# Performance work log

Hardware: AMD Instinct MI355X
Metric: run time of the kernel (lower is better)

The kernel has to match this reference:

```python
import jax, jax.numpy as jnp
import numpy as np

N_TOKEN = 100000
D = 512
CUTOFFS = [10000, 20000, 50000, N_TOKEN]
CUTOFF_ENDS = [0] + CUTOFFS
N_CLUSTERS = 3
SHORTLIST = 10000
HEAD_SIZE = SHORTLIST + N_CLUSTERS  # 10003
CL_ROOT = [5, 17, 123, 10005, 20007, 50011]
# per-cluster relative root indices (predict_root=False masks roots)
CL_ROOT_REL = []
for i in range(len(CUTOFFS)):
    l, r = CUTOFF_ENDS[i], CUTOFF_ENDS[i + 1]
    CL_ROOT_REL.append([j - l for j in CL_ROOT if l <= j < r])


def _mask_cols(logit, idxs):
    if idxs:
        return logit.at[:, jnp.asarray(idxs)].set(-jnp.inf)
    return logit


def setup_inputs() -> dict:
    key = jax.random.key(0)
    ks = jax.random.split(key, 6)
    return {
        "hidden": jax.random.normal(ks[0], (2048, D), dtype=jnp.float32),
        "weight": jax.random.normal(ks[1], (N_TOKEN, D), dtype=jnp.float32) * 0.02,
        "bias": jax.random.normal(ks[2], (N_TOKEN,), dtype=jnp.float32) * 0.02,
        "cluster_weight": jax.random.normal(ks[3], (N_CLUSTERS, D), dtype=jnp.float32) * 0.02,
        "cluster_bias": jax.random.normal(ks[4], (N_CLUSTERS,), dtype=jnp.float32) * 0.02,
        "target": jax.random.randint(ks[5], (2048,), 0, N_TOKEN, dtype=jnp.int64),
    }


def reference(hidden, weight, bias, cluster_weight, cluster_bias, target):
    # head: shortlist vocab rows + cluster rows
    head_w = jnp.concatenate([weight[:SHORTLIST], cluster_weight], axis=0)  # [HEAD_SIZE, D]
    head_b = jnp.concatenate([bias[:SHORTLIST], cluster_bias], axis=0)
    head_logit = hidden @ head_w.T + head_b                                 # [N, HEAD_SIZE]
    head_logit = _mask_cols(head_logit, CL_ROOT_REL[0])
    head_lp = jax.nn.log_softmax(head_logit, axis=1)

    # cluster 0: direct gather from head log-probs
    mask0 = target < CUTOFFS[0]
    t0 = jnp.clip(target, 0, HEAD_SIZE - 1)
    lp0 = jnp.take_along_axis(head_lp, t0[:, None], axis=1)[:, 0]
    nll = jnp.where(mask0, -lp0, jnp.zeros_like(lp0))

    # tail clusters: dense per-cluster logits for all tokens, select by mask
    for i in range(1, len(CUTOFFS)):
        l, r = CUTOFF_ENDS[i], CUTOFF_ENDS[i + 1]
        tail_logit = hidden @ weight[l:r].T + bias[l:r]                     # [N, r-l]
        tail_logit = _mask_cols(tail_logit, CL_ROOT_REL[i])
        tail_lp = jax.nn.log_softmax(tail_logit, axis=1)
        t_i = jnp.clip(target - l, 0, r - l - 1)
        lp_tail = jnp.take_along_axis(tail_lp, t_i[:, None], axis=1)[:, 0]
        # note: torch indexes head column -i, i.e. HEAD_SIZE - i
        lp_i = head_lp[:, HEAD_SIZE - i] + lp_tail
        mask_i = (target >= l) & (target < r)
        nll = jnp.where(mask_i, -lp_i, nll)
    return nll
```

## Files before the change

### kernel.cpp

```cpp
#include <hip/hip_runtime.h>
#include <math.h>

#define NTOK   2048
#define D      512
#define NV     100000
#define LOG2E  1.44269504f

typedef __attribute__((ext_vector_type(8)))  short bf16x8;
typedef __attribute__((ext_vector_type(16))) float f32x16;


#define WS_FRAGS 0u
#define WS_LISTS 8388608u
#define WS_PART  8421376u
#define WS_CUR   14843904u
#define WS_PAD   14843920u
#define WS_CL    14843936u
#define WS_TGT   14868512u
#define WS_ACC   14876704u

__device__ __forceinline__ int cluster_of(int t){
  return (t < 10000) ? 0 : (t < 20000) ? 1 : (t < 50000) ? 2 : 3;
}
__device__ __forceinline__ bool is_root(int c){
  return c==5 || c==17 || c==123 || c==10005 || c==20007 || c==50011;
}
__device__ __forceinline__ unsigned short f2bf(float f){
  unsigned int u = __float_as_uint(f);
  u += 0x7fffu + ((u >> 16) & 1u);
  return (unsigned short)(u >> 16);
}
__device__ __forceinline__ float bf2f(unsigned short u){
  unsigned int v = ((unsigned int)u) << 16;
  return __uint_as_float(v);
}
__device__ __forceinline__ float fexp2(float x){
#if __has_builtin(__builtin_amdgcn_exp2f)
  return __builtin_amdgcn_exp2f(x);
#else
  return exp2f(x);
#endif
}

__global__ void k_token_logits(const float* __restrict__ hidden,
                               const float* __restrict__ weight,
                               const float* __restrict__ bias,
                               const float* __restrict__ cw,
                               const float* __restrict__ cb,
                               const int*   __restrict__ target,
                               float* __restrict__ cl_out,
                               float* __restrict__ tgt_out,
                               int*   __restrict__ lists,
                               int*   __restrict__ cursors)
{
  int wave = threadIdx.x >> 6;
  int lane = threadIdx.x & 63;
  int n = blockIdx.x * 4 + wave;
  if (n >= NTOK) return;
  const float* h = hidden + (size_t)n * D + lane * 8;
  int t = target[n];
  const float* wt = weight + (size_t)t * D + lane * 8;
  float hv[8];
  #pragma unroll
  for (int i = 0; i < 8; ++i) hv[i] = h[i];
  float acc[4] = {0.f, 0.f, 0.f, 0.f};
  #pragma unroll
  for (int j = 0; j < 3; ++j){
    const float* cwj = cw + j * D + lane * 8;
    float s = 0.f;
    #pragma unroll
    for (int i = 0; i < 8; ++i) s += hv[i] * cwj[i];
    acc[j] = s;
  }
  {
    float s = 0.f;
    #pragma unroll
    for (int i = 0; i < 8; ++i) s += hv[i] * wt[i];
    acc[3] = s;
  }
  #pragma unroll
  for (int m = 1; m < 64; m <<= 1){
    #pragma unroll
    for (int j = 0; j < 4; ++j) acc[j] += __shfl_xor(acc[j], m, 64);
  }
  if (lane == 0){
    cl_out[n*3+0] = acc[0] + cb[0];
    cl_out[n*3+1] = acc[1] + cb[1];
    cl_out[n*3+2] = acc[2] + cb[2];
    float tg = acc[3] + bias[t];
    if (is_root(t)) tg = -INFINITY;
    tgt_out[n] = tg;
    lists[n] = n;
    int c = cluster_of(t);
    if (c > 0){
      int pos = atomicAdd(cursors + c, 1);
      lists[c * 2048 + pos] = n;
    }
  }
}

__global__ void k_pad_lists(int* __restrict__ lists, const int* __restrict__ cursors,
                            int* __restrict__ padded)
{
  if (threadIdx.x == 0) padded[0] = NTOK;
  for (int s = 1; s < 4; ++s){
    int c = cursors[s];
    int p = (c + 255) & ~255;
    if (threadIdx.x == 0) padded[s] = p;
    for (int i = c + threadIdx.x; i < p; i += blockDim.x)
      lists[s * 2048 + i] = NTOK;
  }
}

__global__ void k_build_frags(const float* __restrict__ hidden,
                              const int*   __restrict__ lists,
                              const int*   __restrict__ padded,
                              unsigned short* __restrict__ frags)
{
  int tg   = blockIdx.x * 256 + threadIdx.x;
  int seg  = tg >> 16;
  int s    = tg & 65535;
  int lane = s & 63;
  int ks0  = (s >> 6) & 15;
  int mf   = s >> 10;
  int row  = mf * 32 + (lane & 31);
  if (row >= padded[seg]) return;
  int token = lists[seg * 2048 + row];
  #pragma unroll
  for (int p = 0; p < 2; ++p){
    int ks = ks0 + p * 16;
    unsigned int w[4];
    if (token < NTOK){
      const float* h = hidden + (size_t)token * D + ks * 16 + (lane >> 5) * 8;
      #pragma unroll
      for (int i = 0; i < 4; ++i){
        unsigned short lo = f2bf(h[2*i]   * LOG2E);
        unsigned short hi = f2bf(h[2*i+1] * LOG2E);
        w[i] = (unsigned int)lo | ((unsigned int)hi << 16);
      }
    } else {
      w[0] = w[1] = w[2] = w[3] = 0u;
    }
    size_t off = ((size_t)seg * 2048 * 512) + (((size_t)(mf * 32 + ks)) * 64 + lane) * 8;
    uint4 val; val.x = w[0]; val.y = w[1]; val.z = w[2]; val.w = w[3];
    *(uint4*)(frags + off) = val;
  }
}

__device__ __forceinline__ void epi2(const f32x16& a, const f32x16& b, int r0,
                                     int lane, unsigned short* __restrict__ pp)
{
  float s = 0.f;
  #pragma unroll
  for (int r = 0; r < 16; ++r) s += fexp2(a[r]) + fexp2(b[r]);
  s += __shfl_xor(s, 32, 64);
  if (lane < 32)
    pp[r0 + lane] = f2bf(s);
}

__global__ __launch_bounds__(512, 4)
void k_gemm(const unsigned short* __restrict__ frags,
            const float* __restrict__ weight,
            const float* __restrict__ bias,
            const int*   __restrict__ padded,
            unsigned short* __restrict__ partials)
{
  __shared__ unsigned short Bs[528 * 64];

  int bid = blockIdx.x;
  int seg, strip0, colstart, colend;
  if      (bid < 157) { seg = 0; strip0 = 0;    colstart = 0;     colend = 10000;  }
  else if (bid < 314) { seg = 1; strip0 = 157;  colstart = 10000; colend = 20000;  }
  else if (bid < 783) { seg = 2; strip0 = 314;  colstart = 20000; colend = 50000;  }
  else                { seg = 3; strip0 = 783;  colstart = 50000; colend = 100000; }
  int col_base = colstart + (bid - strip0) * 64;

  int tid   = threadIdx.x;
  int wave  = tid >> 6;
  int lane  = tid & 63;
  int hi    = lane >> 5;
  int M = padded[seg];
  const unsigned short* fseg = frags + (size_t)seg * 2048 * 512;
  unsigned short* pp = partials + (size_t)bid * 2048;

  for (int it = 0; it < 16; ++it){
    int id  = it * 512 + tid;
    int col = id >> 7;
    int k0  = (id & 127) * 4;
    int cg  = col_base + col;
    float4 v = make_float4(0.f, 0.f, 0.f, 0.f);
    if (cg < colend) v = *(const float4*)(weight + (size_t)cg * D + k0);
    unsigned int lo  = (unsigned int)f2bf(v.x) | ((unsigned int)f2bf(v.y) << 16);
    unsigned int hi2 = (unsigned int)f2bf(v.z) | ((unsigned int)f2bf(v.w) << 16);
    int ks = k0 >> 4, bhi = (k0 >> 3) & 1, j0 = k0 & 7;
    int off = ks * 2048 + (col >> 5) * 1024 + bhi * 512 + (col & 31) * 16 + j0 * 2;
    off ^= ((ks & 3) << 5) ^ (bhi << 4);
    uint2 pk; pk.x = lo; pk.y = hi2;
    *(uint2*)((char*)Bs + off) = pk;
  }
  if (tid < 256){
    int col = tid >> 2;
    int q   = tid & 3;
    int bhi = q >> 1;
    int j0  = (q & 1) * 4;
    int cg  = col_base + col;
    unsigned int x = 0u;
    if (bhi == 0 && j0 == 0){
      float bv = (cg < colend && !is_root(cg)) ? bias[cg] * LOG2E : -INFINITY;
      x = (unsigned int)f2bf(bv);
    }
    int off = 32 * 2048 + (col >> 5) * 1024 + bhi * 512 + (col & 31) * 16 + j0 * 2;
    off ^= ((32 & 3) << 5) ^ (bhi << 4);
    uint2 pk; pk.x = x; pk.y = 0u;
    *(uint2*)((char*)Bs + off) = pk;
  }
  __syncthreads();

  const char* bsc = (const char*)Bs;
  int roff = (lane * 16) ^ (hi << 4);

  bf16x8 ones;
  #pragma unroll
  for (int j = 0; j < 8; ++j) ones[j] = (short)0x3F80;

  for (int m0 = 0; m0 < M; m0 += 512){
    int r0 = m0 + wave * 64;
    if (r0 < M){
      f32x16 acc00, acc01, acc10, acc11;
      #pragma unroll
      for (int i = 0; i < 16; ++i){ acc00[i]=0.f; acc01[i]=0.f; acc10[i]=0.f; acc11[i]=0.f; }

      const unsigned short* pa0 = fseg + (size_t)(r0 >> 5) * 16384 + (size_t)lane * 8;
      const unsigned short* pa1 = pa0 + 16384;

      __builtin_amdgcn_s_setprio(1);
      #pragma unroll 4
      for (int ks = 0; ks < 32; ++ks){
        bf16x8 a0 = *(const bf16x8*)(pa0 + ks * 512);
        bf16x8 a1 = *(const bf16x8*)(pa1 + ks * 512);
        int kb = ks * 2048 + (roff ^ ((ks & 3) << 5));
        bf16x8 b0 = *(const bf16x8*)(bsc + kb);
        bf16x8 b1 = *(const bf16x8*)(bsc + kb + 1024);
        acc00 = __builtin_amdgcn_mfma_f32_32x32x16_bf16(b0, a0, acc00, 0, 0, 0);
        acc01 = __builtin_amdgcn_mfma_f32_32x32x16_bf16(b1, a0, acc01, 0, 0, 0);
        acc10 = __builtin_amdgcn_mfma_f32_32x32x16_bf16(b0, a1, acc10, 0, 0, 0);
        acc11 = __builtin_amdgcn_mfma_f32_32x32x16_bf16(b1, a1, acc11, 0, 0, 0);
      }
      {
        int kb32 = 32 * 2048 + roff;
        bf16x8 bb0 = *(const bf16x8*)(bsc + kb32);
        bf16x8 bb1 = *(const bf16x8*)(bsc + kb32 + 1024);
        acc00 = __builtin_amdgcn_mfma_f32_32x32x16_bf16(bb0, ones, acc00, 0, 0, 0);
        acc01 = __builtin_amdgcn_mfma_f32_32x32x16_bf16(bb1, ones, acc01, 0, 0, 0);
        acc10 = __builtin_amdgcn_mfma_f32_32x32x16_bf16(bb0, ones, acc10, 0, 0, 0);
        acc11 = __builtin_amdgcn_mfma_f32_32x32x16_bf16(bb1, ones, acc11, 0, 0, 0);
      }
      __builtin_amdgcn_s_setprio(0);
      epi2(acc00, acc01, r0,      lane, pp);
      epi2(acc10, acc11, r0 + 32, lane, pp);
    }
  }
}

__global__ void k_reduce(const unsigned short* __restrict__ partials,
                         const int*   __restrict__ lists,
                         const int*   __restrict__ padded,
                         float* __restrict__ acc_out)
{
  int b   = blockIdx.x;
  int seg = b >> 3;
  int row = (b & 7) * 256 + threadIdx.x;
  if (row >= padded[seg]) return;
  int base, cnt;
  if      (seg == 0){ base = 0;   cnt = 157; }
  else if (seg == 1){ base = 157; cnt = 157; }
  else if (seg == 2){ base = 314; cnt = 469; }
  else              { base = 783; cnt = 782; }
  float s = 0.f;
  int j = 0;
  for (; j + 4 <= cnt; j += 4){
    s += bf2f(partials[(size_t)(base + j    ) * 2048 + row]);
    s += bf2f(partials[(size_t)(base + j + 1) * 2048 + row]);
    s += bf2f(partials[(size_t)(base + j + 2) * 2048 + row]);
    s += bf2f(partials[(size_t)(base + j + 3) * 2048 + row]);
  }
  for (; j < cnt; ++j) s += bf2f(partials[(size_t)(base + j) * 2048 + row]);
  int token = lists[seg * 2048 + row];
  if (token < NTOK) acc_out[seg * 2049 + token] = s;
}

__global__ void k_finalize(const float* __restrict__ accs,
                           const float* __restrict__ cl,
                           const float* __restrict__ tgt,
                           const int*   __restrict__ target,
                           float* __restrict__ out)
{
  int n = blockIdx.x * blockDim.x + threadIdx.x;
  if (n >= NTOK) return;
  int c = cluster_of(target[n]);
  float e0 = __expf(cl[n*3+0]), e1 = __expf(cl[n*3+1]), e2 = __expf(cl[n*3+2]);
  float head_lse = __logf(accs[n] + e0 + e1 + e2);
  float nll;
  if (c == 0){
    nll = head_lse - tgt[n];
  } else {
    float tail_lse = __logf(accs[c * 2049 + n]);
    nll = head_lse + tail_lse - cl[n*3 + (3 - c)] - tgt[n];
  }
  out[n] = nll;
}

extern "C" void kernel_launch(void* const* d_in, const int* in_sizes, int n_in,
                              void* d_out, int out_size, void* d_ws, size_t ws_size,
                              hipStream_t stream)
{
  (void)in_sizes; (void)n_in; (void)out_size; (void)ws_size;
  const float* hidden = (const float*)d_in[0];
  const float* weight = (const float*)d_in[1];
  const float* bias   = (const float*)d_in[2];
  const float* cw     = (const float*)d_in[3];
  const float* cb     = (const float*)d_in[4];
  const int*   target = (const int*)d_in[5];
  float* out = (float*)d_out;
  char*  ws  = (char*)d_ws;

  unsigned short* frags    = (unsigned short*)(ws + WS_FRAGS);
  int*   lists    = (int*)(ws + WS_LISTS);
  unsigned short* partials = (unsigned short*)(ws + WS_PART);
  int*   cursors  = (int*)(ws + WS_CUR);
  int*   padded   = (int*)(ws + WS_PAD);
  float* cl       = (float*)(ws + WS_CL);
  float* tgt      = (float*)(ws + WS_TGT);
  float* acc      = (float*)(ws + WS_ACC);

  hipMemsetAsync(ws + WS_CUR, 0, 16, stream);

  k_token_logits<<<512, 256, 0, stream>>>(hidden, weight, bias, cw, cb, target,
                                          cl, tgt, lists, cursors);
  k_pad_lists   <<<1,   256, 0, stream>>>(lists, cursors, padded);
  k_build_frags <<<1024,256, 0, stream>>>(hidden, lists, padded, frags);
  k_gemm        <<<1565,512, 0, stream>>>(frags, weight, bias, padded, partials);
  k_reduce      <<<32,  256, 0, stream>>>(partials, lists, padded, acc);
  k_finalize    <<<8,   256, 0, stream>>>(acc, cl, tgt, target, out);
}
```

Measured before the change: 226.8 us.

## Switch GEMM operands from bf16 to fp8 e4m3 MFMA

Converts both the hidden-state fragments and the weight tile in shared memory to software-encoded fp8 (e4m3) and uses the fp8 32x32x16 MFMA instead of bf16. This halves the fragment and LDS footprint and is meant to use the higher fp8 matrix throughput. The fragment and LDS layouts are rebuilt without the XOR swizzle, and the masked bias becomes -448 instead of -inf. The risk is a large accuracy loss in the log-sum-exp from fp8 rounding and the finite mask value.

```diff
diff --git a/kernel.cpp b/kernel.cpp
--- a/kernel.cpp
+++ b/kernel.cpp
@@ -6,7 +6,7 @@
 #define NV     100000
 #define LOG2E  1.44269504f
 
-typedef __attribute__((ext_vector_type(8)))  short bf16x8;
+typedef __attribute__((ext_vector_type(2)))  long  long2v;
 typedef __attribute__((ext_vector_type(16))) float f32x16;
 
 
@@ -40,6 +40,23 @@
 #else
   return exp2f(x);
 #endif
+}
+__device__ __forceinline__ unsigned int f2fp8(float x){
+  unsigned int u = __float_as_uint(x);
+  unsigned int s = (u >> 24) & 0x80u;
+  float a = fabsf(x);
+  if (!(a < 448.f)) return s | 0x7Eu;
+  if (a < 0.015625f){
+    int m = __float2int_rn(a * 512.0f);
+    return s | (unsigned int)m;
+  }
+  unsigned int au = u & 0x7FFFFFFFu;
+  au += 0x7FFFFu + ((au >> 20) & 1u);
+  int e = (int)(au >> 23) - 127;
+  unsigned int m = (au >> 20) & 7u;
+  unsigned int enc = ((unsigned int)(e + 7) << 3) | m;
+  if (enc > 0x7Eu) enc = 0x7Eu;
+  return s | enc;
 }
 
 __global__ void k_token_logits(const float* __restrict__ hidden,
@@ -115,36 +132,34 @@
 __global__ void k_build_frags(const float* __restrict__ hidden,
                               const int*   __restrict__ lists,
                               const int*   __restrict__ padded,
-                              unsigned short* __restrict__ frags)
+                              unsigned char* __restrict__ frags)
 {
   int tg   = blockIdx.x * 256 + threadIdx.x;
   int seg  = tg >> 16;
   int s    = tg & 65535;
   int lane = s & 63;
-  int ks0  = (s >> 6) & 15;
+  int kp   = (s >> 6) & 15;
   int mf   = s >> 10;
   int row  = mf * 32 + (lane & 31);
   if (row >= padded[seg]) return;
   int token = lists[seg * 2048 + row];
-  #pragma unroll
-  for (int p = 0; p < 2; ++p){
-    int ks = ks0 + p * 16;
-    unsigned int w[4];
-    if (token < NTOK){
-      const float* h = hidden + (size_t)token * D + ks * 16 + (lane >> 5) * 8;
-      #pragma unroll
-      for (int i = 0; i < 4; ++i){
-        unsigned short lo = f2bf(h[2*i]   * LOG2E);
-        unsigned short hi = f2bf(h[2*i+1] * LOG2E);
-        w[i] = (unsigned int)lo | ((unsigned int)hi << 16);
-      }
-    } else {
-      w[0] = w[1] = w[2] = w[3] = 0u;
+  int hi    = lane >> 5;
+  unsigned int w[4] = {0u, 0u, 0u, 0u};
+  if (token < NTOK){
+    const float* h0 = hidden + (size_t)token * D + 32 * kp + hi * 8;
+    const float* h1 = h0 + 16;
+    #pragma unroll
+    for (int g = 0; g < 2; ++g){
+      unsigned int lo = f2fp8(h0[4*g+0]*LOG2E) | (f2fp8(h0[4*g+1]*LOG2E)<<8)
+                      | (f2fp8(h0[4*g+2]*LOG2E)<<16) | (f2fp8(h0[4*g+3]*LOG2E)<<24);
+      unsigned int hiw= f2fp8(h1[4*g+0]*LOG2E) | (f2fp8(h1[4*g+1]*LOG2E)<<8)
+                      | (f2fp8(h1[4*g+2]*LOG2E)<<16) | (f2fp8(h1[4*g+3]*LOG2E)<<24);
+      w[g] = lo; w[2+g] = hiw;
     }
-    size_t off = ((size_t)seg * 2048 * 512) + (((size_t)(mf * 32 + ks)) * 64 + lane) * 8;
-    uint4 val; val.x = w[0]; val.y = w[1]; val.z = w[2]; val.w = w[3];
-    *(uint4*)(frags + off) = val;
-  }
+  }
+  size_t off = (size_t)seg * 1048576u + (((size_t)(mf * 16 + kp)) * 64 + lane) * 16;
+  uint4 val; val.x = w[0]; val.y = w[1]; val.z = w[2]; val.w = w[3];
+  *(uint4*)(frags + off) = val;
 }
 
 __device__ __forceinline__ void epi2(const f32x16& a, const f32x16& b, int r0,
@@ -159,13 +174,13 @@
 }
 
 __global__ __launch_bounds__(512, 4)
-void k_gemm(const unsigned short* __restrict__ frags,
+void k_gemm(const unsigned char* __restrict__ frags,
             const float* __restrict__ weight,
             const float* __restrict__ bias,
             const int*   __restrict__ padded,
             unsigned short* __restrict__ partials)
 {
-  __shared__ unsigned short Bs[528 * 64];
+  __shared__ unsigned char Bs[34816];
 
   int bid = blockIdx.x;
   int seg, strip0, colstart, colend;
@@ -178,9 +193,8 @@
   int tid   = threadIdx.x;
   int wave  = tid >> 6;
   int lane  = tid & 63;
-  int hi    = lane >> 5;
   int M = padded[seg];
-  const unsigned short* fseg = frags + (size_t)seg * 2048 * 512;
+  const unsigned char* fseg = frags + (size_t)seg * 1048576u;
   unsigned short* pp = partials + (size_t)bid * 2048;
 
   for (int it = 0; it < 16; ++it){
@@ -190,38 +204,30 @@
     int cg  = col_base + col;
     float4 v = make_float4(0.f, 0.f, 0.f, 0.f);
     if (cg < colend) v = *(const float4*)(weight + (size_t)cg * D + k0);
-    unsigned int lo  = (unsigned int)f2bf(v.x) | ((unsigned int)f2bf(v.y) << 16);
-    unsigned int hi2 = (unsigned int)f2bf(v.z) | ((unsigned int)f2bf(v.w) << 16);
-    int ks = k0 >> 4, bhi = (k0 >> 3) & 1, j0 = k0 & 7;
-    int off = ks * 2048 + (col >> 5) * 1024 + bhi * 512 + (col & 31) * 16 + j0 * 2;
-    off ^= ((ks & 3) << 5) ^ (bhi << 4);
-    uint2 pk; pk.x = lo; pk.y = hi2;
-    *(uint2*)((char*)Bs + off) = pk;
-  }
-  if (tid < 256){
-    int col = tid >> 2;
-    int q   = tid & 3;
-    int bhi = q >> 1;
-    int j0  = (q & 1) * 4;
-    int cg  = col_base + col;
+    unsigned int pk = f2fp8(v.x) | (f2fp8(v.y)<<8) | (f2fp8(v.z)<<16) | (f2fp8(v.w)<<24);
+    int ks = k0 >> 4, kp = ks >> 1, ksub = ks & 1, kk = k0 & 15;
+    int hi2 = kk >> 3, j0 = kk & 7;
+    int off = kp * 2048 + (col >> 5) * 1024 + ((col & 31) + 32 * hi2) * 16 + ksub * 8 + j0;
+    *(unsigned int*)(Bs + off) = pk;
+  }
+  if (tid < 128){
+    int col  = tid & 63;
+    int part = tid >> 6;
+    int cg   = col_base + col;
     unsigned int x = 0u;
-    if (bhi == 0 && j0 == 0){
-      float bv = (cg < colend && !is_root(cg)) ? bias[cg] * LOG2E : -INFINITY;
-      x = (unsigned int)f2bf(bv);
+    if (part == 0){
+      float bv = (cg < colend && !is_root(cg)) ? bias[cg] * LOG2E : -448.f;
+      x = f2fp8(bv);
     }
-    int off = 32 * 2048 + (col >> 5) * 1024 + bhi * 512 + (col & 31) * 16 + j0 * 2;
-    off ^= ((32 & 3) << 5) ^ (bhi << 4);
-    uint2 pk; pk.x = x; pk.y = 0u;
-    *(uint2*)((char*)Bs + off) = pk;
+    int off = 32768 + (col >> 5) * 1024 + ((col & 31) + 32 * part) * 16;
+    uint4 z; z.x = x; z.y = 0u; z.z = 0u; z.w = 0u;
+    *(uint4*)(Bs + off) = z;
   }
   __syncthreads();
 
   const char* bsc = (const char*)Bs;
-  int roff = (lane * 16) ^ (hi << 4);
-
-  bf16x8 ones;
-  #pragma unroll
-  for (int j = 0; j < 8; ++j) ones[j] = (short)0x3F80;
+  int l16 = lane * 16;
+  long ones8 = 0x3838383838383838L;
 
   for (int m0 = 0; m0 < M; m0 += 512){
     int r0 = m0 + wave * 64;
@@ -230,30 +236,32 @@
       #pragma unroll
       for (int i = 0; i < 16; ++i){ acc00[i]=0.f; acc01[i]=0.f; acc10[i]=0.f; acc11[i]=0.f; }
 
-      const unsigned short* pa0 = fseg + (size_t)(r0 >> 5) * 16384 + (size_t)lane * 8;
-      const unsigned short* pa1 = pa0 + 16384;
+      const unsigned char* pa0 = fseg + (size_t)(r0 >> 5) * 16384 + (size_t)lane * 16;
+      const unsigned char* pa1 = pa0 + 16384;
 
       __builtin_amdgcn_s_setprio(1);
       #pragma unroll 4
-      for (int ks = 0; ks < 32; ++ks){
-        bf16x8 a0 = *(const bf16x8*)(pa0 + ks * 512);
-        bf16x8 a1 = *(const bf16x8*)(pa1 + ks * 512);
-        int kb = ks * 2048 + (roff ^ ((ks & 3) << 5));
-        bf16x8 b0 = *(const bf16x8*)(bsc + kb);
-        bf16x8 b1 = *(const bf16x8*)(bsc + kb + 1024);
-        acc00 = __builtin_amdgcn_mfma_f32_32x32x16_bf16(b0, a0, acc00, 0, 0, 0);
-        acc01 = __builtin_amdgcn_mfma_f32_32x32x16_bf16(b1, a0, acc01, 0, 0, 0);
-        acc10 = __builtin_amdgcn_mfma_f32_32x32x16_bf16(b0, a1, acc10, 0, 0, 0);
-        acc11 = __builtin_amdgcn_mfma_f32_32x32x16_bf16(b1, a1, acc11, 0, 0, 0);
+      for (int kp = 0; kp < 16; ++kp){
+        long2v A0 = *(const long2v*)(pa0 + kp * 1024);
+        long2v A1 = *(const long2v*)(pa1 + kp * 1024);
+        long2v B0 = *(const long2v*)(bsc + kp * 2048 + l16);
+        long2v B1 = *(const long2v*)(bsc + kp * 2048 + 1024 + l16);
+        acc00 = __builtin_amdgcn_mfma_f32_32x32x16_fp8_fp8(B0[0], A0[0], acc00, 0, 0, 0);
+        acc01 = __builtin_amdgcn_mfma_f32_32x32x16_fp8_fp8(B1[0], A0[0], acc01, 0, 0, 0);
+        acc10 = __builtin_amdgcn_mfma_f32_32x32x16_fp8_fp8(B0[0], A1[0], acc10, 0, 0, 0);
+        acc11 = __builtin_amdgcn_mfma_f32_32x32x16_fp8_fp8(B1[0], A1[0], acc11, 0, 0, 0);
+        acc00 = __builtin_amdgcn_mfma_f32_32x32x16_fp8_fp8(B0[1], A0[1], acc00, 0, 0, 0);
+        acc01 = __builtin_amdgcn_mfma_f32_32x32x16_fp8_fp8(B1[1], A0[1], acc01, 0, 0, 0);
+        acc10 = __builtin_amdgcn_mfma_f32_32x32x16_fp8_fp8(B0[1], A1[1], acc10, 0, 0, 0);
+        acc11 = __builtin_amdgcn_mfma_f32_32x32x16_fp8_fp8(B1[1], A1[1], acc11, 0, 0, 0);
       }
       {
-        int kb32 = 32 * 2048 + roff;
-        bf16x8 bb0 = *(const bf16x8*)(bsc + kb32);
-        bf16x8 bb1 = *(const bf16x8*)(bsc + kb32 + 1024);
-        acc00 = __builtin_amdgcn_mfma_f32_32x32x16_bf16(bb0, ones, acc00, 0, 0, 0);
-        acc01 = __builtin_amdgcn_mfma_f32_32x32x16_bf16(bb1, ones, acc01, 0, 0, 0);
-        acc10 = __builtin_amdgcn_mfma_f32_32x32x16_bf16(bb0, ones, acc10, 0, 0, 0);
-        acc11 = __builtin_amdgcn_mfma_f32_32x32x16_bf16(bb1, ones, acc11, 0, 0, 0);
+        long bb0 = *(const long*)(bsc + 32768 + l16);
+        long bb1 = *(const long*)(bsc + 32768 + 1024 + l16);
+        acc00 = __builtin_amdgcn_mfma_f32_32x32x16_fp8_fp8(bb0, ones8, acc00, 0, 0, 0);
+        acc01 = __builtin_amdgcn_mfma_f32_32x32x16_fp8_fp8(bb1, ones8, acc01, 0, 0, 0);
+        acc10 = __builtin_amdgcn_mfma_f32_32x32x16_fp8_fp8(bb0, ones8, acc10, 0, 0, 0);
+        acc11 = __builtin_amdgcn_mfma_f32_32x32x16_fp8_fp8(bb1, ones8, acc11, 0, 0, 0);
       }
       __builtin_amdgcn_s_setprio(0);
       epi2(acc00, acc01, r0,      lane, pp);
@@ -324,7 +332,7 @@
   float* out = (float*)d_out;
   char*  ws  = (char*)d_ws;
 
-  unsigned short* frags    = (unsigned short*)(ws + WS_FRAGS);
+  unsigned char*  frags    = (unsigned char*)(ws + WS_FRAGS);
   int*   lists    = (int*)(ws + WS_LISTS);
   unsigned short* partials = (unsigned short*)(ws + WS_PART);
   int*   cursors  = (int*)(ws + WS_CUR);
```

Result: no change. 224.0 us (-1.3%).
